# Optimization experiments

Hardware: AMD Instinct MI355X
Metric: run time of the kernel (lower is better)

## Reference

```python
import jax, jax.numpy as jnp
import numpy as np

MIN_SIGMA = 0.1
MAX_SIGMA = 10.0


def _sigma_mlp(e, w1, b1, w2, b2, w3, b3):
    # e: [B, N, E] -> sigma in [min_sigma, max_sigma], shape [B, N, 1]
    h = jax.nn.gelu(e @ w1 + b1, approximate=False)
    h = jax.nn.gelu(h @ w2 + b2, approximate=False)
    s = jax.nn.sigmoid(h @ w3 + b3)
    return MIN_SIGMA + (MAX_SIGMA - MIN_SIGMA) * s


def setup_inputs() -> dict:
    key = jax.random.key(0)
    ks = jax.random.split(key, 9)
    M, P = 2048, 2
    B, N, E = 8, 1024, 256
    H = 32
    z = jax.random.normal(ks[0], (M, P), dtype=jnp.float32)
    mu = jax.random.normal(ks[1], (B, N, P), dtype=jnp.float32)
    embeddings = jax.random.normal(ks[2], (B, N, E), dtype=jnp.float32)
    # sigma-predictor MLP params (torch Linear default-ish init scale)
    w1 = jax.random.normal(ks[3], (E, H), dtype=jnp.float32) / np.sqrt(E)
    b1 = jnp.zeros((H,), dtype=jnp.float32)
    w2 = jax.random.normal(ks[4], (H, H // 2), dtype=jnp.float32) / np.sqrt(H)
    b2 = jnp.zeros((H // 2,), dtype=jnp.float32)
    w3 = jax.random.normal(ks[5], (H // 2, 1), dtype=jnp.float32) / np.sqrt(H // 2)
    b3 = jnp.zeros((1,), dtype=jnp.float32)
    return {"z": z, "mu": mu, "embeddings": embeddings,
            "w1": w1, "b1": b1, "w2": w2, "b2": b2, "w3": w3, "b3": b3}


def reference(z, mu, embeddings, w1, b1, w2, b2, w3, b3):
    # sigma: [B, N, 1]
    sigma = _sigma_mlp(embeddings, w1, b1, w2, b2, w3, b3)
    # squared distances: [B, N, M] = sum_P (z[m,p] - mu[b,n,p])^2
    # z: [M, P], mu: [B, N, P]
    d2 = jnp.sum((z[None, None, :, :] - mu[:, :, None, :]) ** 2, axis=-1)
    # kernel values: [B, N, M]
    return jnp.exp(-d2 / (2.0 * sigma ** 2))
```

## Files before the change

kernel.cpp:

```cpp
#include <hip/hip_runtime.h>
#include <math.h>

#define ROWS 8192
#define M_TOTAL 2048
#define E_DIM 256
#define H1 32
#define H2 16

__device__ __forceinline__ float gelu_exact(float x) {
    return 0.5f * x * (1.0f + erff(x * 0.70710678118654752f));
}

__global__ __launch_bounds__(256) void fused_rbf_kernel(
    const float* __restrict__ z, const float* __restrict__ mu,
    const float* __restrict__ emb,
    const float* __restrict__ w1, const float* __restrict__ b1,
    const float* __restrict__ w2, const float* __restrict__ b2,
    const float* __restrict__ w3, const float* __restrict__ b3,
    float* __restrict__ out)
{
    __shared__ float se[E_DIM];
    __shared__ float red[8][H1];
    __shared__ float h1s[H1];
    __shared__ float h2s[H2];
    __shared__ float csh;

    const int row = blockIdx.x;
    const int t = threadIdx.x;

    se[t] = emb[(size_t)row * E_DIM + t];
    __syncthreads();

    {
        const int o = t & 31;
        const int chunk = t >> 5;
        const int k0 = chunk * 32;
        float acc = 0.f;
        #pragma unroll
        for (int j = 0; j < 32; ++j) {
            const int k = k0 + j;
            acc = fmaf(se[k], w1[k * H1 + o], acc);
        }
        red[chunk][o] = acc;
    }
    __syncthreads();

    if (t < H1) {
        float h = red[0][t] + red[1][t] + red[2][t] + red[3][t]
                + red[4][t] + red[5][t] + red[6][t] + red[7][t];
        h1s[t] = gelu_exact(h + b1[t]);
    }
    __syncthreads();

    if (t < H2) {
        float a = 0.f;
        #pragma unroll
        for (int k = 0; k < H1; ++k) a = fmaf(h1s[k], w2[k * H2 + t], a);
        h2s[t] = gelu_exact(a + b2[t]);
    }
    __syncthreads();

    if (t == 0) {
        float sum = 0.f;
        #pragma unroll
        for (int k = 0; k < H2; ++k) sum = fmaf(h2s[k], w3[k], sum);
        const float x = sum + b3[0];
        const float s = 1.0f / (1.0f + __expf(-x));
        const float sigma = 0.1f + 9.9f * s;
        csh = -0.5f / (sigma * sigma);
    }
    __syncthreads();

    const float c = csh;
    const float mu0 = mu[row * 2 + 0];
    const float mu1 = mu[row * 2 + 1];
    const float4* zf4 = (const float4*)z;
    float4* out4 = (float4*)out + (size_t)row * (M_TOTAL / 4);

    #pragma unroll
    for (int i = 0; i < 2; ++i) {
        const int idx = i * 256 + t;
        const float4 za = zf4[idx * 2 + 0];
        const float4 zb = zf4[idx * 2 + 1];
        float4 r;
        float d0, d1;
        d0 = za.x - mu0; d1 = za.y - mu1;
        r.x = __expf(fmaf(d1, d1, d0 * d0) * c);
        d0 = za.z - mu0; d1 = za.w - mu1;
        r.y = __expf(fmaf(d1, d1, d0 * d0) * c);
        d0 = zb.x - mu0; d1 = zb.y - mu1;
        r.z = __expf(fmaf(d1, d1, d0 * d0) * c);
        d0 = zb.z - mu0; d1 = zb.w - mu1;
        r.w = __expf(fmaf(d1, d1, d0 * d0) * c);
        out4[idx] = r;
    }
}

extern "C" void kernel_launch(void* const* d_in, const int* in_sizes, int n_in,
                              void* d_out, int out_size, void* d_ws, size_t ws_size,
                              hipStream_t stream) {
    const float* z   = (const float*)d_in[0];
    const float* mu  = (const float*)d_in[1];
    const float* emb = (const float*)d_in[2];
    const float* w1  = (const float*)d_in[3];
    const float* b1  = (const float*)d_in[4];
    const float* w2  = (const float*)d_in[5];
    const float* b2  = (const float*)d_in[6];
    const float* w3  = (const float*)d_in[7];
    const float* b3  = (const float*)d_in[8];
    float* out = (float*)d_out;

    fused_rbf_kernel<<<ROWS, 256, 0, stream>>>(z, mu, emb, w1, b1, w2, b2, w3, b3, out);
}
```

Baseline: 107.5 us.

## Split sigma MLP into batched kernel with shared-memory W1 reuse

Moves the sigma MLP into its own kernel that processes 32 rows per block, staging the embeddings and the full W1 in shared memory so each weight is reused across four rows per thread. The per-row coefficient goes to workspace, and a second lightweight kernel computes the RBF output. This removes the per-row W1 reloads and the serial tail phases from the bandwidth-bound output kernel. In exchange it adds a second launch, a workspace round trip, and a 64KB shared-memory footprint that limits occupancy of the MLP kernel.

New measurement: 105.5 us. Within noise of the previous version (-1.9%).

```diff
diff --git a/kernel.cpp b/kernel.cpp
--- a/kernel.cpp
+++ b/kernel.cpp
@@ -6,72 +6,106 @@
 #define E_DIM 256
 #define H1 32
 #define H2 16
+#define R_PER_BLK 32
 
 __device__ __forceinline__ float gelu_exact(float x) {
     return 0.5f * x * (1.0f + erff(x * 0.70710678118654752f));
 }
 
-__global__ __launch_bounds__(256) void fused_rbf_kernel(
-    const float* __restrict__ z, const float* __restrict__ mu,
+__global__ __launch_bounds__(256) void sigma_mlp_v2(
     const float* __restrict__ emb,
     const float* __restrict__ w1, const float* __restrict__ b1,
     const float* __restrict__ w2, const float* __restrict__ b2,
     const float* __restrict__ w3, const float* __restrict__ b3,
-    float* __restrict__ out)
+    float* __restrict__ c_out)
 {
-    __shared__ float se[E_DIM];
-    __shared__ float red[8][H1];
-    __shared__ float h1s[H1];
-    __shared__ float h2s[H2];
-    __shared__ float csh;
+    __shared__ float se[R_PER_BLK * E_DIM];
+    __shared__ float sw1[E_DIM * H1];
+    __shared__ float sh1[R_PER_BLK][H1 + 1];
+    __shared__ float sh2[R_PER_BLK][H2 + 1];
 
-    const int row = blockIdx.x;
     const int t = threadIdx.x;
+    const int row0 = blockIdx.x * R_PER_BLK;
 
-    se[t] = emb[(size_t)row * E_DIM + t];
+    {
+        const float4* src_e = (const float4*)(emb + (size_t)row0 * E_DIM);
+        float4* dst_e = (float4*)se;
+        const float4* src_w = (const float4*)w1;
+        float4* dst_w = (float4*)sw1;
+        #pragma unroll
+        for (int i = 0; i < 8; ++i) {
+            dst_e[t + 256 * i] = src_e[t + 256 * i];
+            dst_w[t + 256 * i] = src_w[t + 256 * i];
+        }
+    }
     __syncthreads();
 
     {
         const int o = t & 31;
-        const int chunk = t >> 5;
-        const int k0 = chunk * 32;
-        float acc = 0.f;
-        #pragma unroll
-        for (int j = 0; j < 32; ++j) {
-            const int k = k0 + j;
-            acc = fmaf(se[k], w1[k * H1 + o], acc);
+        const int g = t >> 5;
+        float acc0 = 0.f, acc1 = 0.f, acc2 = 0.f, acc3 = 0.f;
+        const float4* se4 = (const float4*)se;
+        const int rb = g * 4;
+        for (int k4 = 0; k4 < E_DIM / 4; ++k4) {
+            float4 e0 = se4[(rb + 0) * (E_DIM / 4) + k4];
+            float4 e1 = se4[(rb + 1) * (E_DIM / 4) + k4];
+            float4 e2 = se4[(rb + 2) * (E_DIM / 4) + k4];
+            float4 e3 = se4[(rb + 3) * (E_DIM / 4) + k4];
+            const int k = k4 * 4;
+            float wa = sw1[(k + 0) * H1 + o];
+            float wb = sw1[(k + 1) * H1 + o];
+            float wc = sw1[(k + 2) * H1 + o];
+            float wd = sw1[(k + 3) * H1 + o];
+            acc0 = fmaf(e0.x, wa, acc0); acc0 = fmaf(e0.y, wb, acc0);
+            acc0 = fmaf(e0.z, wc, acc0); acc0 = fmaf(e0.w, wd, acc0);
+            acc1 = fmaf(e1.x, wa, acc1); acc1 = fmaf(e1.y, wb, acc1);
+            acc1 = fmaf(e1.z, wc, acc1); acc1 = fmaf(e1.w, wd, acc1);
+            acc2 = fmaf(e2.x, wa, acc2); acc2 = fmaf(e2.y, wb, acc2);
+            acc2 = fmaf(e2.z, wc, acc2); acc2 = fmaf(e2.w, wd, acc2);
+            acc3 = fmaf(e3.x, wa, acc3); acc3 = fmaf(e3.y, wb, acc3);
+            acc3 = fmaf(e3.z, wc, acc3); acc3 = fmaf(e3.w, wd, acc3);
         }
-        red[chunk][o] = acc;
+        const float bo = b1[o];
+        sh1[rb + 0][o] = gelu_exact(acc0 + bo);
+        sh1[rb + 1][o] = gelu_exact(acc1 + bo);
+        sh1[rb + 2][o] = gelu_exact(acc2 + bo);
+        sh1[rb + 3][o] = gelu_exact(acc3 + bo);
     }
     __syncthreads();
 
-    if (t < H1) {
-        float h = red[0][t] + red[1][t] + red[2][t] + red[3][t]
-                + red[4][t] + red[5][t] + red[6][t] + red[7][t];
-        h1s[t] = gelu_exact(h + b1[t]);
+    {
+        const int o2 = t & 15;
+        const int rr = t >> 4;
+        const float bo = b2[o2];
+        #pragma unroll
+        for (int h = 0; h < 2; ++h) {
+            const int r = rr + 16 * h;
+            float a = 0.f;
+            #pragma unroll
+            for (int k = 0; k < H1; ++k) a = fmaf(sh1[r][k], w2[k * H2 + o2], a);
+            sh2[r][o2] = gelu_exact(a + bo);
+        }
     }
     __syncthreads();
 
-    if (t < H2) {
-        float a = 0.f;
+    if (t < R_PER_BLK) {
+        float s = 0.f;
         #pragma unroll
-        for (int k = 0; k < H1; ++k) a = fmaf(h1s[k], w2[k * H2 + t], a);
-        h2s[t] = gelu_exact(a + b2[t]);
+        for (int k = 0; k < H2; ++k) s = fmaf(sh2[t][k], w3[k], s);
+        const float x = s + b3[0];
+        const float sig = 1.0f / (1.0f + __expf(-x));
+        const float sigma = 0.1f + 9.9f * sig;
+        c_out[row0 + t] = -0.5f / (sigma * sigma);
     }
-    __syncthreads();
+}
 
-    if (t == 0) {
-        float sum = 0.f;
-        #pragma unroll
-        for (int k = 0; k < H2; ++k) sum = fmaf(h2s[k], w3[k], sum);
-        const float x = sum + b3[0];
-        const float s = 1.0f / (1.0f + __expf(-x));
-        const float sigma = 0.1f + 9.9f * s;
-        csh = -0.5f / (sigma * sigma);
-    }
-    __syncthreads();
-
-    const float c = csh;
+__global__ __launch_bounds__(256) void rbf_kernel(
+    const float* __restrict__ z, const float* __restrict__ mu,
+    const float* __restrict__ c_in, float* __restrict__ out)
+{
+    const int row = blockIdx.x;
+    const int t = threadIdx.x;
+    const float c = c_in[row];
     const float mu0 = mu[row * 2 + 0];
     const float mu1 = mu[row * 2 + 1];
     const float4* zf4 = (const float4*)z;
@@ -109,6 +143,8 @@
     const float* w3  = (const float*)d_in[7];
     const float* b3  = (const float*)d_in[8];
     float* out = (float*)d_out;
+    float* c_ws = (float*)d_ws;
 
-    fused_rbf_kernel<<<ROWS, 256, 0, stream>>>(z, mu, emb, w1, b1, w2, b2, w3, b3, out);
+    sigma_mlp_v2<<<ROWS / R_PER_BLK, 256, 0, stream>>>(emb, w1, b1, w2, b2, w3, b3, c_ws);
+    rbf_kernel<<<ROWS, 256, 0, stream>>>(z, mu, c_ws, out);
 }
```

## Assign one wavefront per row, compute sigma MLP with shuffles, stage z in LDS

Applied to the files above, without the earlier changes.

Each 256-thread block now handles four rows, one per 64-lane wavefront. The sigma MLP runs entirely inside a wave using shuffles instead of shared-memory reductions and several block barriers. z is loaded once per block into shared memory, de-interleaved into x and y arrays, and reused across the four rows. This removes most serial single-thread MLP work and barrier stalls, but each lane now does more of the embedding dot product and the block uses 16KB of LDS.

Measured after the change: 112.1 us. 4.3% more time.

```diff
diff --git a/kernel.cpp b/kernel.cpp
--- a/kernel.cpp
+++ b/kernel.cpp
@@ -11,7 +11,7 @@
     return 0.5f * x * (1.0f + erff(x * 0.70710678118654752f));
 }
 
-__global__ __launch_bounds__(256) void fused_rbf_kernel(
+__global__ __launch_bounds__(256) void fused_rbf_v2(
     const float* __restrict__ z, const float* __restrict__ mu,
     const float* __restrict__ emb,
     const float* __restrict__ w1, const float* __restrict__ b1,
@@ -19,80 +19,83 @@
     const float* __restrict__ w3, const float* __restrict__ b3,
     float* __restrict__ out)
 {
-    __shared__ float se[E_DIM];
-    __shared__ float red[8][H1];
-    __shared__ float h1s[H1];
-    __shared__ float h2s[H2];
-    __shared__ float csh;
+    __shared__ float szx[M_TOTAL];
+    __shared__ float szy[M_TOTAL];
 
-    const int row = blockIdx.x;
     const int t = threadIdx.x;
+    const int wave = t >> 6;
+    const int l = t & 63;
+    const int row = blockIdx.x * 4 + wave;
 
-    se[t] = emb[(size_t)row * E_DIM + t];
+    {
+        const float4* z4 = (const float4*)z;
+        #pragma unroll
+        for (int i = 0; i < 4; ++i) {
+            const int p = t + 256 * i;
+            const float4 v = z4[p];
+            szx[2 * p]     = v.x; szy[2 * p]     = v.y;
+            szx[2 * p + 1] = v.z; szy[2 * p + 1] = v.w;
+        }
+    }
+
+    const int o = l & 31;
+    const int half = l >> 5;
+    float acc = 0.f;
+    {
+        const float4* e4 = (const float4*)(emb + (size_t)row * E_DIM + half * 128);
+        const float* w1p = w1 + (size_t)(half * 128) * H1 + o;
+        #pragma unroll 8
+        for (int k4 = 0; k4 < 32; ++k4) {
+            const float4 ev = e4[k4];
+            acc = fmaf(ev.x, w1p[(4 * k4 + 0) * H1], acc);
+            acc = fmaf(ev.y, w1p[(4 * k4 + 1) * H1], acc);
+            acc = fmaf(ev.z, w1p[(4 * k4 + 2) * H1], acc);
+            acc = fmaf(ev.w, w1p[(4 * k4 + 3) * H1], acc);
+        }
+    }
+    float h1v = acc + __shfl_xor(acc, 32);
+    h1v = gelu_exact(h1v + b1[o]);
+
+    const int o2 = l & 15;
+    float acc2 = 0.f;
+    #pragma unroll
+    for (int k = 0; k < H1; ++k)
+        acc2 = fmaf(__shfl(h1v, k), w2[k * H2 + o2], acc2);
+    const float h2v = gelu_exact(acc2 + b2[o2]);
+
+    float t3 = h2v * w3[o2];
+    t3 += __shfl_xor(t3, 1);
+    t3 += __shfl_xor(t3, 2);
+    t3 += __shfl_xor(t3, 4);
+    t3 += __shfl_xor(t3, 8);
+    const float x = t3 + b3[0];
+    const float sig = 1.0f / (1.0f + __expf(-x));
+    const float sigma = 0.1f + 9.9f * sig;
+    const float c = -0.5f / (sigma * sigma);
+
+    const float2 muv = ((const float2*)mu)[row];
+
     __syncthreads();
 
-    {
-        const int o = t & 31;
-        const int chunk = t >> 5;
-        const int k0 = chunk * 32;
-        float acc = 0.f;
-        #pragma unroll
-        for (int j = 0; j < 32; ++j) {
-            const int k = k0 + j;
-            acc = fmaf(se[k], w1[k * H1 + o], acc);
-        }
-        red[chunk][o] = acc;
-    }
-    __syncthreads();
-
-    if (t < H1) {
-        float h = red[0][t] + red[1][t] + red[2][t] + red[3][t]
-                + red[4][t] + red[5][t] + red[6][t] + red[7][t];
-        h1s[t] = gelu_exact(h + b1[t]);
-    }
-    __syncthreads();
-
-    if (t < H2) {
-        float a = 0.f;
-        #pragma unroll
-        for (int k = 0; k < H1; ++k) a = fmaf(h1s[k], w2[k * H2 + t], a);
-        h2s[t] = gelu_exact(a + b2[t]);
-    }
-    __syncthreads();
-
-    if (t == 0) {
-        float sum = 0.f;
-        #pragma unroll
-        for (int k = 0; k < H2; ++k) sum = fmaf(h2s[k], w3[k], sum);
-        const float x = sum + b3[0];
-        const float s = 1.0f / (1.0f + __expf(-x));
-        const float sigma = 0.1f + 9.9f * s;
-        csh = -0.5f / (sigma * sigma);
-    }
-    __syncthreads();
-
-    const float c = csh;
-    const float mu0 = mu[row * 2 + 0];
-    const float mu1 = mu[row * 2 + 1];
-    const float4* zf4 = (const float4*)z;
-    float4* out4 = (float4*)out + (size_t)row * (M_TOTAL / 4);
-
+    const float4* szx4 = (const float4*)szx;
+    const float4* szy4 = (const float4*)szy;
+    float4* o4 = (float4*)out + (size_t)row * (M_TOTAL / 4);
     #pragma unroll
-    for (int i = 0; i < 2; ++i) {
-        const int idx = i * 256 + t;
-        const float4 za = zf4[idx * 2 + 0];
-        const float4 zb = zf4[idx * 2 + 1];
-        float4 r;
-        float d0, d1;
-        d0 = za.x - mu0; d1 = za.y - mu1;
-        r.x = __expf(fmaf(d1, d1, d0 * d0) * c);
-        d0 = za.z - mu0; d1 = za.w - mu1;
-        r.y = __expf(fmaf(d1, d1, d0 * d0) * c);
-        d0 = zb.x - mu0; d1 = zb.y - mu1;
-        r.z = __expf(fmaf(d1, d1, d0 * d0) * c);
-        d0 = zb.z - mu0; d1 = zb.w - mu1;
-        r.w = __expf(fmaf(d1, d1, d0 * d0) * c);
-        out4[idx] = r;
+    for (int i = 0; i < 8; ++i) {
+        const int j = i * 64 + l;
+        const float4 zx = szx4[j];
+        const float4 zy = szy4[j];
+        float4 v;
+        float dx, dy;
+        dx = zx.x - muv.x; dy = zy.x - muv.y;
+        v.x = __expf(fmaf(dy, dy, dx * dx) * c);
+        dx = zx.y - muv.x; dy = zy.y - muv.y;
+        v.y = __expf(fmaf(dy, dy, dx * dx) * c);
+        dx = zx.z - muv.x; dy = zy.z - muv.y;
+        v.z = __expf(fmaf(dy, dy, dx * dx) * c);
+        dx = zx.w - muv.x; dy = zy.w - muv.y;
+        v.w = __expf(fmaf(dy, dy, dx * dx) * c);
+        o4[j] = v;
     }
 }
 
@@ -110,5 +113,5 @@
     const float* b3  = (const float*)d_in[8];
     float* out = (float*)d_out;
 
-    fused_rbf_kernel<<<ROWS, 256, 0, stream>>>(z, mu, emb, w1, b1, w2, b2, w3, b3, out);
+    fused_rbf_v2<<<ROWS / 4, 256, 0, stream>>>(z, mu, emb, w1, b1, w2, b2, w3, b3, out);
 }
```
